# Kernel optimization log

Hardware: AMD Instinct MI355X
Metric: run time of the kernel (lower is better)

## Reference

```python
import jax, jax.numpy as jnp
import numpy as np

KERNEL_SIZE = 5
GROUP_SIZE = 1
SCALE = 2


def setup_inputs() -> dict:
    key = jax.random.key(0)
    k1, k2 = jax.random.split(key)
    N, C, H, W = 2, 256, 100, 100
    features = jax.random.normal(k1, (N, C, H, W), dtype=jnp.float32)
    masks = jax.random.uniform(
        k2, (N, KERNEL_SIZE * KERNEL_SIZE * GROUP_SIZE, H * SCALE, W * SCALE),
        dtype=jnp.float32)
    return {"features": features, "masks": masks}


def _carafe_naive(features, masks, k, g, s):
    N, C, H, W = features.shape
    r = (k - 1) // 2
    # zero-pad spatially, then gather the k*k neighborhood of every low-res pixel
    pad = jnp.pad(features, ((0, 0), (0, 0), (r, r), (r, r)))
    # patches: [N, C, k*k, H, W] -- fixed small loop over k*k shifts
    patches = jnp.stack(
        [pad[:, :, dy:dy + H, dx:dx + W] for dy in range(k) for dx in range(k)],
        axis=2)
    cg = C // g
    # masks: [N, g, k*k, H, s, W, s]  (output pixel (h*s+a, w*s+b))
    m = masks.reshape(N, g, k * k, H, s, W, s)
    # patches per group: [N, g, cg, k*k, H, W]
    p = patches.reshape(N, g, cg, k * k, H, W)
    # weighted sum over the k*k window; result [N, g, cg, H, s, W, s]
    out = jnp.einsum('ngkhawb,ngckhw->ngchawb', m, p)
    return out.reshape(N, C, H * s, W * s)


def reference(features, masks):
    return _carafe_naive(features, masks, KERNEL_SIZE, GROUP_SIZE, SCALE)
```

## Files before the change

### kernel.cpp

```cpp
#include <hip/hip_runtime.h>


typedef float v2f __attribute__((ext_vector_type(2)));

#define N_ 2
#define C_ 256
#define H_ 100
#define W_ 100
#define CC 8
#define HW_ (H_ * W_)
#define OW_ (W_ * 2)
#define OHW_ (HW_ * 4)
#define NCHUNK (C_ / CC)
#define TW 25
#define TH 10
#define HX 29
#define NROW 28
#define RSTR 29
#define TILES_X (W_ / TW)
#define TILES_Y (H_ / TH)
#define TILES (TILES_X * TILES_Y)

__global__ __launch_bounds__(256) void carafe_kernel(
    const float* __restrict__ feat,
    const float* __restrict__ mask,
    float* __restrict__ out) {

    __shared__ float4 lds4[NROW * RSTR];

    const int cchunk = blockIdx.x;
    const int tile   = blockIdx.y;
    const int n      = blockIdx.z;
    const int tx = tile % TILES_X;
    const int ty = tile / TILES_X;
    const int x0 = tx * TW;
    const int y0 = ty * TH;
    const int t = threadIdx.x;
    const int lane = t & 31;
    const int g = t >> 5;

    {
        const float* fb = feat + (n * C_ + cchunk * CC) * HW_;
        const int xx = x0 - 2 + lane;
        const bool xok = (lane < HX) & ((unsigned)xx < (unsigned)W_);
#pragma unroll
        for (int r = 0; r < 4; ++r) {
            const int p = g * 4 + r;
            const int y = p >> 1;
            const int cq = p & 1;
            const int yy = y0 - 2 + y;
            float v0 = 0.f, v1 = 0.f, v2 = 0.f, v3 = 0.f;
            if (xok & ((unsigned)yy < (unsigned)H_) & (p < NROW)) {
                const int o = (cq * 4) * HW_ + yy * W_ + xx;
                v0 = fb[o];
                v1 = fb[o + HW_];
                v2 = fb[o + 2 * HW_];
                v3 = fb[o + 3 * HW_];
            }
            if ((p < NROW) & (lane < HX))
                lds4[p * RSTR + lane] = make_float4(v0, v1, v2, v3);
        }
    }
    __syncthreads();

    if (t >= TH * TW) return;
    const int hl = t / TW;
    const int wl = t % TW;

    v2f a0[CC], a1[CC];
#pragma unroll
    for (int c = 0; c < CC; ++c) { a0[c] = (v2f){0.f, 0.f}; a1[c] = (v2f){0.f, 0.f}; }

    const int oh0 = 2 * (y0 + hl);
    const int ow0 = 2 * (x0 + wl);
    const float* mbase = mask + n * (25 * OHW_) + oh0 * OW_ + ow0;

#pragma unroll 2
    for (int dy = 0; dy < 5; ++dy) {
        const int ry = (hl + dy) * 2;
        const float* mrow_dy = mbase + (dy * 5) * OHW_;
#pragma unroll
        for (int dx = 0; dx < 5; ++dx) {
            const v2f m0 = *reinterpret_cast<const v2f*>(mrow_dy + dx * OHW_);
            const v2f m1 = *reinterpret_cast<const v2f*>(mrow_dy + dx * OHW_ + OW_);
            const float4 lo = lds4[ry * RSTR + wl + dx];
            const float4 hi = lds4[(ry + 1) * RSTR + wl + dx];
            const float f[8] = {lo.x, lo.y, lo.z, lo.w, hi.x, hi.y, hi.z, hi.w};
#pragma unroll
            for (int c = 0; c < CC; ++c) {
                const v2f fv = {f[c], f[c]};
                a0[c] = __builtin_elementwise_fma(fv, m0, a0[c]);
                a1[c] = __builtin_elementwise_fma(fv, m1, a1[c]);
            }
        }
    }

    float* ob = out + (n * C_ + cchunk * CC) * OHW_ + oh0 * OW_ + ow0;
#pragma unroll
    for (int c = 0; c < CC; ++c) {
        *reinterpret_cast<v2f*>(ob + c * OHW_) = a0[c];
        *reinterpret_cast<v2f*>(ob + c * OHW_ + OW_) = a1[c];
    }
}

extern "C" void kernel_launch(void* const* d_in, const int* in_sizes, int n_in,
                              void* d_out, int out_size, void* d_ws, size_t ws_size,
                              hipStream_t stream) {
    const float* feat = (const float*)d_in[0];
    const float* mask = (const float*)d_in[1];
    float* out = (float*)d_out;

    dim3 grid(NCHUNK, TILES, N_);
    carafe_kernel<<<grid, 256, 0, stream>>>(feat, mask, out);
}
```

Baseline: 38.08 us.

## Process two channel chunks per block with double-buffered LDS prefetch

Each block now handles two 8-channel chunks, halving the grid. The second chunk's features are loaded into registers before the first chunk's compute runs, then written to a second LDS buffer, so global load latency overlaps with FMA work. The cost is half as many blocks (less parallelism and occupancy slack), double the LDS, and a dy loop changed to unroll 1.

```diff
diff --git a/kernel.cpp b/kernel.cpp
--- a/kernel.cpp
+++ b/kernel.cpp
@@ -11,7 +11,7 @@
 #define HW_ (H_ * W_)
 #define OW_ (W_ * 2)
 #define OHW_ (HW_ * 4)
-#define NCHUNK (C_ / CC)
+#define NCPAIR 16
 #define TW 25
 #define TH 10
 #define HX 29
@@ -26,11 +26,11 @@
     const float* __restrict__ mask,
     float* __restrict__ out) {
 
-    __shared__ float4 lds4[NROW * RSTR];
+    __shared__ float4 lds4[2][NROW * RSTR];
 
-    const int cchunk = blockIdx.x;
-    const int tile   = blockIdx.y;
-    const int n      = blockIdx.z;
+    const int cpair = blockIdx.x;
+    const int tile  = blockIdx.y;
+    const int n     = blockIdx.z;
     const int tx = tile % TILES_X;
     const int ty = tile / TILES_X;
     const int x0 = tx * TW;
@@ -39,68 +39,104 @@
     const int lane = t & 31;
     const int g = t >> 5;
 
-    {
-        const float* fb = feat + (n * C_ + cchunk * CC) * HW_;
-        const int xx = x0 - 2 + lane;
-        const bool xok = (lane < HX) & ((unsigned)xx < (unsigned)W_);
-#pragma unroll
-        for (int r = 0; r < 4; ++r) {
-            const int p = g * 4 + r;
-            const int y = p >> 1;
-            const int cq = p & 1;
-            const int yy = y0 - 2 + y;
-            float v0 = 0.f, v1 = 0.f, v2 = 0.f, v3 = 0.f;
-            if (xok & ((unsigned)yy < (unsigned)H_) & (p < NROW)) {
-                const int o = (cq * 4) * HW_ + yy * W_ + xx;
-                v0 = fb[o];
-                v1 = fb[o + HW_];
-                v2 = fb[o + 2 * HW_];
-                v3 = fb[o + 3 * HW_];
-            }
-            if ((p < NROW) & (lane < HX))
-                lds4[p * RSTR + lane] = make_float4(v0, v1, v2, v3);
-        }
-    }
-    __syncthreads();
-
-    if (t >= TH * TW) return;
     const int hl = t / TW;
     const int wl = t % TW;
-
-    v2f a0[CC], a1[CC];
-#pragma unroll
-    for (int c = 0; c < CC; ++c) { a0[c] = (v2f){0.f, 0.f}; a1[c] = (v2f){0.f, 0.f}; }
-
     const int oh0 = 2 * (y0 + hl);
     const int ow0 = 2 * (x0 + wl);
     const float* mbase = mask + n * (25 * OHW_) + oh0 * OW_ + ow0;
+    const bool comp = (t < TH * TW);
 
-#pragma unroll 2
-    for (int dy = 0; dy < 5; ++dy) {
-        const int ry = (hl + dy) * 2;
-        const float* mrow_dy = mbase + (dy * 5) * OHW_;
-#pragma unroll
-        for (int dx = 0; dx < 5; ++dx) {
-            const v2f m0 = *reinterpret_cast<const v2f*>(mrow_dy + dx * OHW_);
-            const v2f m1 = *reinterpret_cast<const v2f*>(mrow_dy + dx * OHW_ + OW_);
-            const float4 lo = lds4[ry * RSTR + wl + dx];
-            const float4 hi = lds4[(ry + 1) * RSTR + wl + dx];
-            const float f[8] = {lo.x, lo.y, lo.z, lo.w, hi.x, hi.y, hi.z, hi.w};
-#pragma unroll
-            for (int c = 0; c < CC; ++c) {
-                const v2f fv = {f[c], f[c]};
-                a0[c] = __builtin_elementwise_fma(fv, m0, a0[c]);
-                a1[c] = __builtin_elementwise_fma(fv, m1, a1[c]);
-            }
-        }
-    }
+    const int xx = x0 - 2 + lane;
+    const bool xok = (lane < HX) & ((unsigned)xx < (unsigned)W_);
 
-    float* ob = out + (n * C_ + cchunk * CC) * OHW_ + oh0 * OW_ + ow0;
-#pragma unroll
-    for (int c = 0; c < CC; ++c) {
-        *reinterpret_cast<v2f*>(ob + c * OHW_) = a0[c];
-        *reinterpret_cast<v2f*>(ob + c * OHW_ + OW_) = a1[c];
-    }
+#define LOADC(chunk, SR)                                                      \
+    do {                                                                      \
+        const float* fb_ = feat + (n * C_ + (chunk) * CC) * HW_;              \
+        _Pragma("unroll")                                                     \
+        for (int r = 0; r < 4; ++r) {                                         \
+            const int p_ = g * 4 + r;                                         \
+            const int yy_ = y0 - 2 + (p_ >> 1);                               \
+            float4 v_ = make_float4(0.f, 0.f, 0.f, 0.f);                      \
+            if (xok & ((unsigned)yy_ < (unsigned)H_) & (p_ < NROW)) {         \
+                const int o_ = ((p_ & 1) * 4) * HW_ + yy_ * W_ + xx;          \
+                v_.x = fb_[o_];                                               \
+                v_.y = fb_[o_ + HW_];                                         \
+                v_.z = fb_[o_ + 2 * HW_];                                     \
+                v_.w = fb_[o_ + 3 * HW_];                                     \
+            }                                                                 \
+            SR[r] = v_;                                                       \
+        }                                                                     \
+    } while (0)
+
+#define WRITEB(buf, SR)                                                       \
+    do {                                                                      \
+        _Pragma("unroll")                                                     \
+        for (int r = 0; r < 4; ++r) {                                         \
+            const int p_ = g * 4 + r;                                         \
+            if ((p_ < NROW) & (lane < HX))                                    \
+                (buf)[p_ * RSTR + lane] = SR[r];                              \
+        }                                                                     \
+    } while (0)
+
+#define COMPUTE(buf, chunk)                                                   \
+    do {                                                                      \
+        if (comp) {                                                           \
+            v2f a0_[CC], a1_[CC];                                             \
+            _Pragma("unroll")                                                 \
+            for (int c = 0; c < CC; ++c) {                                    \
+                a0_[c] = (v2f){0.f, 0.f};                                     \
+                a1_[c] = (v2f){0.f, 0.f};                                     \
+            }                                                                 \
+            _Pragma("unroll 1")                                               \
+            for (int dy = 0; dy < 5; ++dy) {                                  \
+                const int ry_ = (hl + dy) * 2;                                \
+                const float* mr_ = mbase + (dy * 5) * OHW_;                   \
+                _Pragma("unroll")                                             \
+                for (int dx = 0; dx < 5; ++dx) {                              \
+                    const v2f m0_ = *reinterpret_cast<const v2f*>(mr_ + dx * OHW_);       \
+                    const v2f m1_ = *reinterpret_cast<const v2f*>(mr_ + dx * OHW_ + OW_); \
+                    const float4 lo_ = (buf)[ry_ * RSTR + wl + dx];           \
+                    const float4 hi_ = (buf)[(ry_ + 1) * RSTR + wl + dx];     \
+                    const float f_[8] = {lo_.x, lo_.y, lo_.z, lo_.w,          \
+                                         hi_.x, hi_.y, hi_.z, hi_.w};         \
+                    _Pragma("unroll")                                         \
+                    for (int c = 0; c < CC; ++c) {                            \
+                        const v2f fv_ = {f_[c], f_[c]};                       \
+                        a0_[c] = __builtin_elementwise_fma(fv_, m0_, a0_[c]); \
+                        a1_[c] = __builtin_elementwise_fma(fv_, m1_, a1_[c]); \
+                    }                                                         \
+                }                                                             \
+            }                                                                 \
+            float* ob_ = out + (n * C_ + (chunk) * CC) * OHW_ + oh0 * OW_ + ow0; \
+            _Pragma("unroll")                                                 \
+            for (int c = 0; c < CC; ++c) {                                    \
+                *reinterpret_cast<v2f*>(ob_ + c * OHW_) = a0_[c];             \
+                *reinterpret_cast<v2f*>(ob_ + c * OHW_ + OW_) = a1_[c];       \
+            }                                                                 \
+        }                                                                     \
+    } while (0)
+
+    const int cA = cpair * 2;
+    const int cB = cpair * 2 + 1;
+
+    float4 srA[4], srB[4];
+
+    LOADC(cA, srA);
+    WRITEB(lds4[0], srA);
+    __syncthreads();
+
+    LOADC(cB, srB);
+    __builtin_amdgcn_sched_barrier(0);
+    COMPUTE(lds4[0], cA);
+    __builtin_amdgcn_sched_barrier(0);
+    WRITEB(lds4[1], srB);
+    __syncthreads();
+
+    COMPUTE(lds4[1], cB);
+
+#undef LOADC
+#undef WRITEB
+#undef COMPUTE
 }
 
 extern "C" void kernel_launch(void* const* d_in, const int* in_sizes, int n_in,
@@ -110,6 +146,6 @@
     const float* mask = (const float*)d_in[1];
     float* out = (float*)d_out;
 
-    dim3 grid(NCHUNK, TILES, N_);
+    dim3 grid(NCPAIR, TILES, N_);
     carafe_kernel<<<grid, 256, 0, stream>>>(feat, mask, out);
 }
```

Measured after the change: 43.26 us. +13.6%, slower.

## Switch to 16x16 square spatial tiles with full thread use and nontemporal stores

Applied to the files above, without the earlier changes.

Replaces the 25x10 tiles (250 of 256 threads active) with 16x16 tiles covering a 7x7 grid. Every thread now computes a pixel, with clamped mask reads and a guard on the output store for out-of-range pixels. The halo load becomes a flat cooperative loop over a 20-wide, 40-row LDS tile. Output writes use nontemporal stores to avoid polluting the cache. The trade-off is wasted work on the partial edge tiles (112 covered vs 100 needed), a smaller halo ratio per tile, and a different wave mapping of mask reads (16-wide rows instead of 25-wide).

```diff
diff --git a/kernel.cpp b/kernel.cpp
--- a/kernel.cpp
+++ b/kernel.cpp
@@ -12,14 +12,12 @@
 #define OW_ (W_ * 2)
 #define OHW_ (HW_ * 4)
 #define NCHUNK (C_ / CC)
-#define TW 25
-#define TH 10
-#define HX 29
-#define NROW 28
-#define RSTR 29
-#define TILES_X (W_ / TW)
-#define TILES_Y (H_ / TH)
-#define TILES (TILES_X * TILES_Y)
+#define TS 16
+#define HS 20
+#define NROW 40
+#define RSTR 21
+#define NT7 7
+#define TILES (NT7 * NT7)
 
 __global__ __launch_bounds__(256) void carafe_kernel(
     const float* __restrict__ feat,
@@ -31,58 +29,60 @@
     const int cchunk = blockIdx.x;
     const int tile   = blockIdx.y;
     const int n      = blockIdx.z;
-    const int tx = tile % TILES_X;
-    const int ty = tile / TILES_X;
-    const int x0 = tx * TW;
-    const int y0 = ty * TH;
+    const int tx = tile % NT7;
+    const int ty = tile / NT7;
+    const int x0 = tx * TS;
+    const int y0 = ty * TS;
     const int t = threadIdx.x;
-    const int lane = t & 31;
-    const int g = t >> 5;
 
     {
         const float* fb = feat + (n * C_ + cchunk * CC) * HW_;
-        const int xx = x0 - 2 + lane;
-        const bool xok = (lane < HX) & ((unsigned)xx < (unsigned)W_);
 #pragma unroll
         for (int r = 0; r < 4; ++r) {
-            const int p = g * 4 + r;
-            const int y = p >> 1;
-            const int cq = p & 1;
-            const int yy = y0 - 2 + y;
-            float v0 = 0.f, v1 = 0.f, v2 = 0.f, v3 = 0.f;
-            if (xok & ((unsigned)yy < (unsigned)H_) & (p < NROW)) {
-                const int o = (cq * 4) * HW_ + yy * W_ + xx;
-                v0 = fb[o];
-                v1 = fb[o + HW_];
-                v2 = fb[o + 2 * HW_];
-                v3 = fb[o + 3 * HW_];
+            const int i = r * 256 + t;
+            if (i < NROW * HS) {
+                const int row = i / HS;
+                const int col = i % HS;
+                const int y  = row >> 1;
+                const int cq = row & 1;
+                const int yy = y0 - 2 + y;
+                const int xx = x0 - 2 + col;
+                float4 v = make_float4(0.f, 0.f, 0.f, 0.f);
+                if (((unsigned)yy < (unsigned)H_) & ((unsigned)xx < (unsigned)W_)) {
+                    const int o = (cq * 4) * HW_ + yy * W_ + xx;
+                    v.x = fb[o];
+                    v.y = fb[o + HW_];
+                    v.z = fb[o + 2 * HW_];
+                    v.w = fb[o + 3 * HW_];
+                }
+                lds4[row * RSTR + col] = v;
             }
-            if ((p < NROW) & (lane < HX))
-                lds4[p * RSTR + lane] = make_float4(v0, v1, v2, v3);
         }
     }
     __syncthreads();
 
-    if (t >= TH * TW) return;
-    const int hl = t / TW;
-    const int wl = t % TW;
+    const int py = t >> 4;
+    const int wl = t & 15;
+    const int h = y0 + py;
+    const int w = x0 + wl;
+    const bool alive = (h < H_) & (w < W_);
+    const int hc = min(h, H_ - 1), wc = min(w, W_ - 1);
+    const int oh0 = 2 * hc;
+    const int ow0 = 2 * wc;
+    const float* mbase = mask + n * (25 * OHW_) + oh0 * OW_ + ow0;
 
     v2f a0[CC], a1[CC];
 #pragma unroll
     for (int c = 0; c < CC; ++c) { a0[c] = (v2f){0.f, 0.f}; a1[c] = (v2f){0.f, 0.f}; }
 
-    const int oh0 = 2 * (y0 + hl);
-    const int ow0 = 2 * (x0 + wl);
-    const float* mbase = mask + n * (25 * OHW_) + oh0 * OW_ + ow0;
-
 #pragma unroll 2
     for (int dy = 0; dy < 5; ++dy) {
-        const int ry = (hl + dy) * 2;
-        const float* mrow_dy = mbase + (dy * 5) * OHW_;
+        const int ry = (py + dy) * 2;
+        const float* mrow = mbase + (dy * 5) * OHW_;
 #pragma unroll
         for (int dx = 0; dx < 5; ++dx) {
-            const v2f m0 = *reinterpret_cast<const v2f*>(mrow_dy + dx * OHW_);
-            const v2f m1 = *reinterpret_cast<const v2f*>(mrow_dy + dx * OHW_ + OW_);
+            const v2f m0 = *reinterpret_cast<const v2f*>(mrow + dx * OHW_);
+            const v2f m1 = *reinterpret_cast<const v2f*>(mrow + dx * OHW_ + OW_);
             const float4 lo = lds4[ry * RSTR + wl + dx];
             const float4 hi = lds4[(ry + 1) * RSTR + wl + dx];
             const float f[8] = {lo.x, lo.y, lo.z, lo.w, hi.x, hi.y, hi.z, hi.w};
@@ -95,11 +95,13 @@
         }
     }
 
-    float* ob = out + (n * C_ + cchunk * CC) * OHW_ + oh0 * OW_ + ow0;
+    if (alive) {
+        float* ob = out + (n * C_ + cchunk * CC) * OHW_ + oh0 * OW_ + ow0;
 #pragma unroll
-    for (int c = 0; c < CC; ++c) {
-        *reinterpret_cast<v2f*>(ob + c * OHW_) = a0[c];
-        *reinterpret_cast<v2f*>(ob + c * OHW_ + OW_) = a1[c];
+        for (int c = 0; c < CC; ++c) {
+            __builtin_nontemporal_store(a0[c], reinterpret_cast<v2f*>(ob + c * OHW_));
+            __builtin_nontemporal_store(a1[c], reinterpret_cast<v2f*>(ob + c * OHW_ + OW_));
+        }
     }
 }
 
```

Result: slower. 54.18 us (+42.3%).

## Pre-transpose features to channel-interleaved layout and drop LDS staging

Applied to the files above, without the earlier changes.

Adds a separate transpose kernel that writes the features into a workspace with each group of 8 channels interleaved per pixel as two float4 values. The main kernel drops the shared-memory halo tile and __syncthreads, and reads the 5x5 neighbourhood straight from global memory with clamped indices, zeroing the mask weights for out-of-range taps. The goal is to remove the LDS fill and barrier, but it adds a second kernel launch, a full extra pass that reads and writes the features, and relies on cache for neighbour reuse. If the workspace is too small, a fallback does strided per-channel global loads.

```diff
diff --git a/kernel.cpp b/kernel.cpp
--- a/kernel.cpp
+++ b/kernel.cpp
@@ -2,90 +2,92 @@
 
 
 typedef float v2f __attribute__((ext_vector_type(2)));
+typedef float v4f __attribute__((ext_vector_type(4)));
 
 #define N_ 2
 #define C_ 256
 #define H_ 100
 #define W_ 100
-#define CC 8
 #define HW_ (H_ * W_)
 #define OW_ (W_ * 2)
 #define OHW_ (HW_ * 4)
+#define CC 8
 #define NCHUNK (C_ / CC)
 #define TW 25
 #define TH 10
-#define HX 29
-#define NROW 28
-#define RSTR 29
 #define TILES_X (W_ / TW)
 #define TILES_Y (H_ / TH)
 #define TILES (TILES_X * TILES_Y)
+#define FT_ELEMS (N_ * NCHUNK * HW_ * 2)
+#define FT_BYTES ((size_t)FT_ELEMS * 16)
 
-__global__ __launch_bounds__(256) void carafe_kernel(
-    const float* __restrict__ feat,
-    const float* __restrict__ mask,
-    float* __restrict__ out) {
+__global__ __launch_bounds__(256) void transpose_kernel(
+    const float* __restrict__ feat, v4f* __restrict__ ft) {
+    const int i = blockIdx.x * 256 + threadIdx.x;
+    if (i >= FT_ELEMS) return;
+    const int q   = i & 1;
+    const int tmp = i >> 1;
+    const int yx  = tmp % HW_;
+    const int nc  = tmp / HW_;
+    const float* fb = feat + (nc * CC + q * 4) * HW_ + yx;
+    v4f v = { fb[0], fb[HW_], fb[2 * HW_], fb[3 * HW_] };
+    ft[i] = v;
+}
 
-    __shared__ float4 lds4[NROW * RSTR];
+template <bool USE_FT>
+__global__ __launch_bounds__(256) void carafe_main(
+    const v4f* __restrict__ ft, const float* __restrict__ feat,
+    const float* __restrict__ mask, float* __restrict__ out) {
 
-    const int cchunk = blockIdx.x;
-    const int tile   = blockIdx.y;
-    const int n      = blockIdx.z;
+    const int cg   = blockIdx.x;
+    const int tile = blockIdx.y;
+    const int n    = blockIdx.z;
     const int tx = tile % TILES_X;
     const int ty = tile / TILES_X;
-    const int x0 = tx * TW;
-    const int y0 = ty * TH;
+    const int x0 = tx * TW, y0 = ty * TH;
     const int t = threadIdx.x;
-    const int lane = t & 31;
-    const int g = t >> 5;
+    if (t >= TH * TW) return;
+    const int hl = t / TW, wl = t % TW;
+    const int h = y0 + hl, w = x0 + wl;
+    const int oh0 = 2 * h, ow0 = 2 * w;
 
-    {
-        const float* fb = feat + (n * C_ + cchunk * CC) * HW_;
-        const int xx = x0 - 2 + lane;
-        const bool xok = (lane < HX) & ((unsigned)xx < (unsigned)W_);
-#pragma unroll
-        for (int r = 0; r < 4; ++r) {
-            const int p = g * 4 + r;
-            const int y = p >> 1;
-            const int cq = p & 1;
-            const int yy = y0 - 2 + y;
-            float v0 = 0.f, v1 = 0.f, v2 = 0.f, v3 = 0.f;
-            if (xok & ((unsigned)yy < (unsigned)H_) & (p < NROW)) {
-                const int o = (cq * 4) * HW_ + yy * W_ + xx;
-                v0 = fb[o];
-                v1 = fb[o + HW_];
-                v2 = fb[o + 2 * HW_];
-                v3 = fb[o + 3 * HW_];
-            }
-            if ((p < NROW) & (lane < HX))
-                lds4[p * RSTR + lane] = make_float4(v0, v1, v2, v3);
-        }
-    }
-    __syncthreads();
-
-    if (t >= TH * TW) return;
-    const int hl = t / TW;
-    const int wl = t % TW;
+    const float* mbase = mask + n * (25 * OHW_) + oh0 * OW_ + ow0;
+    const v4f* fb = ft + (size_t)(n * NCHUNK + cg) * (HW_ * 2);
+    const float* fs = feat + (n * C_ + cg * CC) * HW_;
 
     v2f a0[CC], a1[CC];
 #pragma unroll
     for (int c = 0; c < CC; ++c) { a0[c] = (v2f){0.f, 0.f}; a1[c] = (v2f){0.f, 0.f}; }
 
-    const int oh0 = 2 * (y0 + hl);
-    const int ow0 = 2 * (x0 + wl);
-    const float* mbase = mask + n * (25 * OHW_) + oh0 * OW_ + ow0;
-
 #pragma unroll 2
     for (int dy = 0; dy < 5; ++dy) {
-        const int ry = (hl + dy) * 2;
-        const float* mrow_dy = mbase + (dy * 5) * OHW_;
+        const int y = h + dy - 2;
+        const bool yv = (unsigned)y < (unsigned)H_;
+        const int yc = min(max(y, 0), H_ - 1);
+        const float* mrow = mbase + (dy * 5) * OHW_;
 #pragma unroll
         for (int dx = 0; dx < 5; ++dx) {
-            const v2f m0 = *reinterpret_cast<const v2f*>(mrow_dy + dx * OHW_);
-            const v2f m1 = *reinterpret_cast<const v2f*>(mrow_dy + dx * OHW_ + OW_);
-            const float4 lo = lds4[ry * RSTR + wl + dx];
-            const float4 hi = lds4[(ry + 1) * RSTR + wl + dx];
-            const float f[8] = {lo.x, lo.y, lo.z, lo.w, hi.x, hi.y, hi.z, hi.w};
+            const int x = w + dx - 2;
+            const bool v = yv && ((unsigned)x < (unsigned)W_);
+            const int xc = min(max(x, 0), W_ - 1);
+
+            v2f m0 = *reinterpret_cast<const v2f*>(mrow + dx * OHW_);
+            v2f m1 = *reinterpret_cast<const v2f*>(mrow + dx * OHW_ + OW_);
+            if (!v) { m0 = (v2f){0.f, 0.f}; m1 = (v2f){0.f, 0.f}; }
+
+            float f[8];
+            if (USE_FT) {
+                const int fo = (yc * W_ + xc) * 2;
+                const v4f lo = fb[fo];
+                const v4f hi = fb[fo + 1];
+                f[0] = lo.x; f[1] = lo.y; f[2] = lo.z; f[3] = lo.w;
+                f[4] = hi.x; f[5] = hi.y; f[6] = hi.z; f[7] = hi.w;
+            } else {
+                const int fo = yc * W_ + xc;
+#pragma unroll
+                for (int c = 0; c < CC; ++c) f[c] = fs[c * HW_ + fo];
+            }
+
 #pragma unroll
             for (int c = 0; c < CC; ++c) {
                 const v2f fv = {f[c], f[c]};
@@ -95,7 +97,7 @@
         }
     }
 
-    float* ob = out + (n * C_ + cchunk * CC) * OHW_ + oh0 * OW_ + ow0;
+    float* ob = out + (n * C_ + cg * CC) * OHW_ + oh0 * OW_ + ow0;
 #pragma unroll
     for (int c = 0; c < CC; ++c) {
         *reinterpret_cast<v2f*>(ob + c * OHW_) = a0[c];
@@ -111,5 +113,13 @@
     float* out = (float*)d_out;
 
     dim3 grid(NCHUNK, TILES, N_);
-    carafe_kernel<<<grid, 256, 0, stream>>>(feat, mask, out);
+
+    if (ws_size >= FT_BYTES) {
+        v4f* ft = (v4f*)d_ws;
+        const int tp_blocks = (FT_ELEMS + 255) / 256;
+        transpose_kernel<<<tp_blocks, 256, 0, stream>>>(feat, ft);
+        carafe_main<true><<<grid, 256, 0, stream>>>(ft, feat, mask, out);
+    } else {
+        carafe_main<false><<<grid, 256, 0, stream>>>(nullptr, feat, mask, out);
+    }
 }
```

Result: slower. 61.70 us (+62.0%).
